# Performance work log

Measured on AMD Instinct MI355X. Metric: run time of the kernel, lower is better.

The kernel has to match this reference:

```python
import jax, jax.numpy as jnp
import numpy as np

HEAD_DIM = 128
SCALE = HEAD_DIM ** -0.5  # head_scaling == up_scaling == 1/sqrt(head_dim)


def setup_inputs() -> dict:
    key = jax.random.key(0)
    kq, kk, ku, kv = jax.random.split(key, 4)
    B, H, S, D = 2, 16, 2048, 128
    Hk, I = 4, 2048
    Q = jax.random.normal(kq, (B, H, S, D), dtype=jnp.float32)
    K = jax.random.normal(kk, (Hk, I, D), dtype=jnp.float32)
    U = jax.random.normal(ku, (Hk, I, D), dtype=jnp.float32)
    V = jax.random.normal(kv, (Hk, I, D), dtype=jnp.float32)
    return {"Q": Q, "K": K, "U": U, "V": V}


def reference(Q, K, U, V):
    # Q: (B, H, S, D); K/U/V: (Hk, I, D); GQA grouping G = H // Hk
    B, H, S, D = Q.shape
    Hk, I, _ = K.shape
    G = H // Hk
    Qr = Q.reshape(B, Hk, G, S, D)
    # gate scores and up projection, both scaled by 1/sqrt(D)
    M = jnp.einsum('bkgsd,kid->bkgsi', Qr, K) * SCALE
    N = jnp.einsum('bkgsd,kid->bkgsi', Qr, U) * SCALE
    A = jax.nn.silu(M) * N  # gated activation, (B, Hk, G, S, I)
    out = jnp.einsum('bkgsi,kid->bkgsd', A, V)
    return out.reshape(B, H, S, D)
```

## Files before the change

### kernel.cpp

```cpp
#include <hip/hip_runtime.h>

#define B_   2
#define H_   16
#define G_   4
#define S_   2048
#define D_   128
#define I_   2048

#define BM   256
#define BN   64
#define TPB  512
#define NIT  (I_ / BN)
#define TSZ  8192

#define KIDX(r,c) ((r)*128 + ((c) ^ (((r)&15)<<3)))
#define VIDX(d,c) ((d)*64  + ((c) ^ (((d)&7)<<3)))

static constexpr float SCALE = 0.08838834764831845f;

typedef __fp16   p2v  __attribute__((ext_vector_type(2)));
typedef _Float16 h8v  __attribute__((ext_vector_type(8)));
typedef float    f4v  __attribute__((ext_vector_type(4)));
typedef float    f16v __attribute__((ext_vector_type(16)));
typedef int      i4v  __attribute__((ext_vector_type(4)));

__device__ __forceinline__ int pkf16(float a, float b) {
    p2v t = __builtin_amdgcn_cvt_pkrtz(a, b);
    int r; __builtin_memcpy(&r, &t, 4); return r;
}

#define GL_LDS(gp, lp) __builtin_amdgcn_global_load_lds(                      \
    (const __attribute__((address_space(1))) void*)(gp),                      \
    (__attribute__((address_space(3))) void*)(lp), 16, 0, 0)

__global__ __launch_bounds__(256) void convert_kernel(
    const float* __restrict__ Kg, const float* __restrict__ Ug,
    const float* __restrict__ Vg, _Float16* __restrict__ ws)
{
    const int bid = blockIdx.x;
    const int tid = threadIdx.x;
    __shared__ float vt[64 * 128];
    if (bid < 256) {
        const int kh = bid >> 6, m = (bid >> 5) & 1, it = bid & 31;
        const float* src = (m ? Ug : Kg) + (size_t)kh * I_ * D_ + (size_t)it * BN * D_;
        _Float16* dst = ws + (((size_t)kh * 3 + m) * 32 + it) * TSZ;
        const int r   = tid >> 2;
        const int cb  = (tid & 3) * 32;
        const int swz = (r & 15) << 3;
#pragma unroll
        for (int g = 0; g < 4; ++g) {
            const int cc0 = cb + g * 8;
            const int d0  = cc0 ^ swz;
            const float4 a = *(const float4*)(src + r * D_ + d0);
            const float4 c = *(const float4*)(src + r * D_ + d0 + 4);
            h8v v; p2v* v2 = (p2v*)&v;
            v2[0] = __builtin_amdgcn_cvt_pkrtz(a.x, a.y);
            v2[1] = __builtin_amdgcn_cvt_pkrtz(a.z, a.w);
            v2[2] = __builtin_amdgcn_cvt_pkrtz(c.x, c.y);
            v2[3] = __builtin_amdgcn_cvt_pkrtz(c.z, c.w);
            *(h8v*)(dst + r * 128 + cc0) = v;
        }
    } else {
        const int v  = bid - 256;
        const int kh = v >> 5, it = v & 31;
        const float* src = Vg + (size_t)kh * I_ * D_ + (size_t)it * BN * D_;
#pragma unroll
        for (int p = 0; p < 8; ++p) {
            const int idx = p * 256 + tid;
            const int i   = idx >> 5;
            const int d4  = (idx & 31) * 4;
            *(float4*)(&vt[i * 128 + d4]) = *(const float4*)(src + (size_t)i * D_ + d4);
        }
        __syncthreads();
        _Float16* dst = ws + (((size_t)kh * 3 + 2) * 32 + it) * TSZ;
        const int d   = tid >> 1;
        const int cb  = (tid & 1) * 32;
        const int swz = (d & 7) << 3;
#pragma unroll
        for (int g = 0; g < 4; ++g) {
            const int cc0 = cb + g * 8;
            const int ib  = cc0 ^ swz;
            h8v w; p2v* w2 = (p2v*)&w;
#pragma unroll
            for (int pr = 0; pr < 4; ++pr)
                w2[pr] = __builtin_amdgcn_cvt_pkrtz(vt[(ib + 2 * pr) * 128 + d],
                                                    vt[(ib + 2 * pr + 1) * 128 + d]);
            *(h8v*)(dst + d * 64 + cc0) = w;
        }
    }
}

__global__ __launch_bounds__(TPB, 2) void flashmlp_kernel(
    const float* __restrict__ Qg, const _Float16* __restrict__ ws,
    float* __restrict__ Og)
{
    __shared__ _Float16 Ks[2 * TSZ];
    __shared__ _Float16 Us[2 * TSZ];
    __shared__ _Float16 Vt[2 * TSZ];

    const int bid   = blockIdx.x;
    const int xcd   = bid & 7;
    const int kh    = xcd >> 1;
    const int j     = ((bid >> 3) << 1) | (xcd & 1);
    const int stile = j & 7;
    const int bg    = j >> 3;
    const int b     = bg >> 2;
    const int g     = bg & 3;
    const int h     = kh * G_ + g;

    const int tid  = threadIdx.x;
    const int wave = tid >> 6;
    const int lane = tid & 63;
    const int l31  = lane & 31;
    const int hl   = lane >> 5;

    const size_t qbase = ((size_t)(b * H_ + h) * S_ + (size_t)stile * BM) * D_;
    const _Float16* wsK = ws + (size_t)kh * 3 * 32 * TSZ;
    const _Float16* wsU = wsK + (size_t)32 * TSZ;
    const _Float16* wsV = wsK + (size_t)64 * TSZ;

    const int so = wave * 1024 + lane * 8;
    const int su = wave * 1024;

    h8v qf[8];
    {
        const float* qp = Qg + qbase + (size_t)(wave * 32 + l31) * D_;
#pragma unroll
        for (int ks = 0; ks < 8; ++ks) {
            const float4 a = *(const float4*)(qp + ks * 16 + hl * 8);
            const float4 c = *(const float4*)(qp + ks * 16 + hl * 8 + 4);
            h8v v; p2v* v2 = (p2v*)&v;
            v2[0] = __builtin_amdgcn_cvt_pkrtz(a.x * SCALE, a.y * SCALE);
            v2[1] = __builtin_amdgcn_cvt_pkrtz(a.z * SCALE, a.w * SCALE);
            v2[2] = __builtin_amdgcn_cvt_pkrtz(c.x * SCALE, c.y * SCALE);
            v2[3] = __builtin_amdgcn_cvt_pkrtz(c.z * SCALE, c.w * SCALE);
            qf[ks] = v;
        }
    }

    f16v acc_o[4];
#pragma unroll
    for (int dt = 0; dt < 4; ++dt)
#pragma unroll
        for (int e = 0; e < 16; ++e)
            acc_o[dt][e] = 0.f;

    {
        GL_LDS(wsK + so,       Ks + su);
        GL_LDS(wsK + so + 512, Ks + su + 512);
        GL_LDS(wsU + so,       Us + su);
        GL_LDS(wsU + so + 512, Us + su + 512);
        GL_LDS(wsV + so,       Vt + su);
        GL_LDS(wsV + so + 512, Vt + su + 512);
    }
    __syncthreads();

    for (int it = 0; it < NIT; ++it) {
        const int cur = it & 1;
        const _Float16* ksb = Ks + cur * TSZ;
        const _Float16* usb = Us + cur * TSZ;
        const _Float16* vtb = Vt + cur * TSZ;

        if (it + 1 < NIT) {
            const int nb = (cur ^ 1) * TSZ;
            const _Float16* kt = wsK + (size_t)(it + 1) * TSZ;
            const _Float16* ut = wsU + (size_t)(it + 1) * TSZ;
            const _Float16* vt = wsV + (size_t)(it + 1) * TSZ;
            GL_LDS(kt + so,       Ks + nb + su);
            GL_LDS(kt + so + 512, Ks + nb + su + 512);
            GL_LDS(ut + so,       Us + nb + su);
            GL_LDS(ut + so + 512, Us + nb + su + 512);
            GL_LDS(vt + so,       Vt + nb + su);
            GL_LDS(vt + so + 512, Vt + nb + su + 512);
        }

#pragma unroll
        for (int t2 = 0; t2 < 2; ++t2) {
            f16v am, an;
#pragma unroll
            for (int e = 0; e < 16; ++e) { am[e] = 0.f; an[e] = 0.f; }
            __builtin_amdgcn_s_setprio(1);
#pragma unroll
            for (int ks = 0; ks < 8; ++ks) {
                const h8v kf = *(const h8v*)(&ksb[KIDX(t2 * 32 + l31, ks * 16 + hl * 8)]);
                const h8v uf = *(const h8v*)(&usb[KIDX(t2 * 32 + l31, ks * 16 + hl * 8)]);
                am = __builtin_amdgcn_mfma_f32_32x32x16_f16(kf, qf[ks], am, 0, 0, 0);
                an = __builtin_amdgcn_mfma_f32_32x32x16_f16(uf, qf[ks], an, 0, 0, 0);
            }
            __builtin_amdgcn_s_setprio(0);

            int P[8];
#pragma unroll
            for (int p = 0; p < 8; ++p) {
                const float m0 = am[2 * p + 0], n0 = an[2 * p + 0];
                const float m1 = am[2 * p + 1], n1 = an[2 * p + 1];
                const float g0 = m0 * __builtin_amdgcn_rcpf(1.f + __expf(-m0)) * n0;
                const float g1 = m1 * __builtin_amdgcn_rcpf(1.f + __expf(-m1)) * n1;
                P[p] = pkf16(g0, g1);
            }
            auto sA = __builtin_amdgcn_permlane32_swap(P[0], P[2], false, false);
            auto sB = __builtin_amdgcn_permlane32_swap(P[1], P[3], false, false);
            auto sC = __builtin_amdgcn_permlane32_swap(P[4], P[6], false, false);
            auto sD = __builtin_amdgcn_permlane32_swap(P[5], P[7], false, false);
            h8v pb0, pb1;
            {
                i4v wlo = i4v{static_cast<int>(sA[0]), static_cast<int>(sB[0]),
                              static_cast<int>(sA[1]), static_cast<int>(sB[1])};
                i4v whi = i4v{static_cast<int>(sC[0]), static_cast<int>(sD[0]),
                              static_cast<int>(sC[1]), static_cast<int>(sD[1])};
                __builtin_memcpy(&pb0, &wlo, 16);
                __builtin_memcpy(&pb1, &whi, 16);
            }

#pragma unroll
            for (int k2 = 0; k2 < 2; ++k2) {
                const int ks2 = t2 * 2 + k2;
                const h8v pb = k2 ? pb1 : pb0;
                h8v va[4];
#pragma unroll
                for (int dt = 0; dt < 4; ++dt)
                    va[dt] = *(const h8v*)(&vtb[VIDX(dt * 32 + l31, ks2 * 16 + hl * 8)]);
                __builtin_amdgcn_s_setprio(1);
#pragma unroll
                for (int dt = 0; dt < 4; ++dt)
                    acc_o[dt] = __builtin_amdgcn_mfma_f32_32x32x16_f16(va[dt], pb, acc_o[dt], 0, 0, 0);
                __builtin_amdgcn_s_setprio(0);
            }
        }

        __syncthreads();
    }

    {
        const int qrow = stile * BM + wave * 32 + l31;
        float* op = Og + ((size_t)(b * H_ + h) * S_ + qrow) * D_;
#pragma unroll
        for (int dt = 0; dt < 4; ++dt)
#pragma unroll
            for (int g4 = 0; g4 < 4; ++g4) {
                f4v v = f4v{acc_o[dt][4 * g4 + 0], acc_o[dt][4 * g4 + 1],
                            acc_o[dt][4 * g4 + 2], acc_o[dt][4 * g4 + 3]};
                *(f4v*)(op + dt * 32 + g4 * 8 + hl * 4) = v;
            }
    }
}

extern "C" void kernel_launch(void* const* d_in, const int* in_sizes, int n_in,
                              void* d_out, int out_size, void* d_ws, size_t ws_size,
                              hipStream_t stream) {
    const float* Q = (const float*)d_in[0];
    const float* K = (const float*)d_in[1];
    const float* U = (const float*)d_in[2];
    const float* V = (const float*)d_in[3];
    float* out = (float*)d_out;
    _Float16* ws = (_Float16*)d_ws;

    convert_kernel<<<dim3(384), dim3(256), 0, stream>>>(K, U, V, ws);
    flashmlp_kernel<<<dim3((S_ / BM) * B_ * H_), dim3(TPB), 0, stream>>>(Q, ws, out);
}
```

Measured before the change: 197.6 us.

## Halve block tiles and split K/U and V pipelines at different granularities

```diff
diff --git a/kernel.cpp b/kernel.cpp
--- a/kernel.cpp
+++ b/kernel.cpp
@@ -7,11 +7,13 @@
 #define D_   128
 #define I_   2048
 
-#define BM   256
-#define BN   64
-#define TPB  512
+#define BM   128
+#define BN   32
+#define TPB  256
 #define NIT  (I_ / BN)
-#define TSZ  8192
+#define KUT  4096
+#define VT   8192
+#define HSTR (3 * 262144)
 
 #define KIDX(r,c) ((r)*128 + ((c) ^ (((r)&15)<<3)))
 #define VIDX(d,c) ((d)*64  + ((c) ^ (((d)&7)<<3)))
@@ -42,11 +44,12 @@
     __shared__ float vt[64 * 128];
     if (bid < 256) {
         const int kh = bid >> 6, m = (bid >> 5) & 1, it = bid & 31;
-        const float* src = (m ? Ug : Kg) + (size_t)kh * I_ * D_ + (size_t)it * BN * D_;
-        _Float16* dst = ws + (((size_t)kh * 3 + m) * 32 + it) * TSZ;
+        const float* src = (m ? Ug : Kg) + (size_t)kh * I_ * D_ + (size_t)it * 64 * D_;
+        _Float16* dstb = ws + (size_t)kh * HSTR + (size_t)m * 262144 + (size_t)it * 2 * KUT;
         const int r   = tid >> 2;
         const int cb  = (tid & 3) * 32;
         const int swz = (r & 15) << 3;
+        _Float16* dst = dstb + (size_t)(r >> 5) * KUT + (r & 31) * 128;
 #pragma unroll
         for (int g = 0; g < 4; ++g) {
             const int cc0 = cb + g * 8;
@@ -58,12 +61,12 @@
             v2[1] = __builtin_amdgcn_cvt_pkrtz(a.z, a.w);
             v2[2] = __builtin_amdgcn_cvt_pkrtz(c.x, c.y);
             v2[3] = __builtin_amdgcn_cvt_pkrtz(c.z, c.w);
-            *(h8v*)(dst + r * 128 + cc0) = v;
+            *(h8v*)(dst + cc0) = v;
         }
     } else {
         const int v  = bid - 256;
         const int kh = v >> 5, it = v & 31;
-        const float* src = Vg + (size_t)kh * I_ * D_ + (size_t)it * BN * D_;
+        const float* src = Vg + (size_t)kh * I_ * D_ + (size_t)it * 64 * D_;
 #pragma unroll
         for (int p = 0; p < 8; ++p) {
             const int idx = p * 256 + tid;
@@ -72,7 +75,7 @@
             *(float4*)(&vt[i * 128 + d4]) = *(const float4*)(src + (size_t)i * D_ + d4);
         }
         __syncthreads();
-        _Float16* dst = ws + (((size_t)kh * 3 + 2) * 32 + it) * TSZ;
+        _Float16* dst = ws + (size_t)kh * HSTR + 2 * 262144 + (size_t)it * VT;
         const int d   = tid >> 1;
         const int cb  = (tid & 1) * 32;
         const int swz = (d & 7) << 3;
@@ -94,16 +97,16 @@
     const float* __restrict__ Qg, const _Float16* __restrict__ ws,
     float* __restrict__ Og)
 {
-    __shared__ _Float16 Ks[2 * TSZ];
-    __shared__ _Float16 Us[2 * TSZ];
-    __shared__ _Float16 Vt[2 * TSZ];
+    __shared__ _Float16 Ks[2 * KUT];
+    __shared__ _Float16 Us[2 * KUT];
+    __shared__ _Float16 Vt[2 * VT];
 
     const int bid   = blockIdx.x;
     const int xcd   = bid & 7;
     const int kh    = xcd >> 1;
     const int j     = ((bid >> 3) << 1) | (xcd & 1);
-    const int stile = j & 7;
-    const int bg    = j >> 3;
+    const int stile = j & 15;
+    const int bg    = j >> 4;
     const int b     = bg >> 2;
     const int g     = bg & 3;
     const int h     = kh * G_ + g;
@@ -115,12 +118,14 @@
     const int hl   = lane >> 5;
 
     const size_t qbase = ((size_t)(b * H_ + h) * S_ + (size_t)stile * BM) * D_;
-    const _Float16* wsK = ws + (size_t)kh * 3 * 32 * TSZ;
-    const _Float16* wsU = wsK + (size_t)32 * TSZ;
-    const _Float16* wsV = wsK + (size_t)64 * TSZ;
-
-    const int so = wave * 1024 + lane * 8;
-    const int su = wave * 1024;
+    const _Float16* wsK = ws + (size_t)kh * HSTR;
+    const _Float16* wsU = wsK + 262144;
+    const _Float16* wsV = wsK + 2 * 262144;
+
+    const int soK = wave * 1024 + lane * 8;
+    const int suK = wave * 1024;
+    const int soV = wave * 2048 + lane * 8;
+    const int suV = wave * 2048;
 
     h8v qf[8];
     {
@@ -146,86 +151,90 @@
             acc_o[dt][e] = 0.f;
 
     {
-        GL_LDS(wsK + so,       Ks + su);
-        GL_LDS(wsK + so + 512, Ks + su + 512);
-        GL_LDS(wsU + so,       Us + su);
-        GL_LDS(wsU + so + 512, Us + su + 512);
-        GL_LDS(wsV + so,       Vt + su);
-        GL_LDS(wsV + so + 512, Vt + su + 512);
+        GL_LDS(wsK + soK,       Ks + suK);
+        GL_LDS(wsK + soK + 512, Ks + suK + 512);
+        GL_LDS(wsU + soK,       Us + suK);
+        GL_LDS(wsU + soK + 512, Us + suK + 512);
+        GL_LDS(wsV + soV,        Vt + suV);
+        GL_LDS(wsV + soV + 512,  Vt + suV + 512);
+        GL_LDS(wsV + soV + 1024, Vt + suV + 1024);
+        GL_LDS(wsV + soV + 1536, Vt + suV + 1536);
     }
     __syncthreads();
 
     for (int it = 0; it < NIT; ++it) {
-        const int cur = it & 1;
-        const _Float16* ksb = Ks + cur * TSZ;
-        const _Float16* usb = Us + cur * TSZ;
-        const _Float16* vtb = Vt + cur * TSZ;
+        const _Float16* ksb = Ks + (it & 1) * KUT;
+        const _Float16* usb = Us + (it & 1) * KUT;
+        const _Float16* vtb = Vt + ((it >> 1) & 1) * VT;
 
         if (it + 1 < NIT) {
-            const int nb = (cur ^ 1) * TSZ;
-            const _Float16* kt = wsK + (size_t)(it + 1) * TSZ;
-            const _Float16* ut = wsU + (size_t)(it + 1) * TSZ;
-            const _Float16* vt = wsV + (size_t)(it + 1) * TSZ;
-            GL_LDS(kt + so,       Ks + nb + su);
-            GL_LDS(kt + so + 512, Ks + nb + su + 512);
-            GL_LDS(ut + so,       Us + nb + su);
-            GL_LDS(ut + so + 512, Us + nb + su + 512);
-            GL_LDS(vt + so,       Vt + nb + su);
-            GL_LDS(vt + so + 512, Vt + nb + su + 512);
-        }
-
-#pragma unroll
-        for (int t2 = 0; t2 < 2; ++t2) {
-            f16v am, an;
-#pragma unroll
-            for (int e = 0; e < 16; ++e) { am[e] = 0.f; an[e] = 0.f; }
+            const int nb = ((it + 1) & 1) * KUT;
+            const _Float16* kt = wsK + (size_t)(it + 1) * KUT;
+            const _Float16* ut = wsU + (size_t)(it + 1) * KUT;
+            GL_LDS(kt + soK,       Ks + nb + suK);
+            GL_LDS(kt + soK + 512, Ks + nb + suK + 512);
+            GL_LDS(ut + soK,       Us + nb + suK);
+            GL_LDS(ut + soK + 512, Us + nb + suK + 512);
+        }
+        if (!(it & 1) && (it >> 1) + 1 < 32) {
+            const int vb = (it >> 1) + 1;
+            const _Float16* vt = wsV + (size_t)vb * VT;
+            const int nv = (vb & 1) * VT;
+            GL_LDS(vt + soV,        Vt + nv + suV);
+            GL_LDS(vt + soV + 512,  Vt + nv + suV + 512);
+            GL_LDS(vt + soV + 1024, Vt + nv + suV + 1024);
+            GL_LDS(vt + soV + 1536, Vt + nv + suV + 1536);
+        }
+
+        f16v am, an;
+#pragma unroll
+        for (int e = 0; e < 16; ++e) { am[e] = 0.f; an[e] = 0.f; }
+        __builtin_amdgcn_s_setprio(1);
+#pragma unroll
+        for (int ks = 0; ks < 8; ++ks) {
+            const h8v kf = *(const h8v*)(&ksb[KIDX(l31, ks * 16 + hl * 8)]);
+            const h8v uf = *(const h8v*)(&usb[KIDX(l31, ks * 16 + hl * 8)]);
+            am = __builtin_amdgcn_mfma_f32_32x32x16_f16(kf, qf[ks], am, 0, 0, 0);
+            an = __builtin_amdgcn_mfma_f32_32x32x16_f16(uf, qf[ks], an, 0, 0, 0);
+        }
+        __builtin_amdgcn_s_setprio(0);
+
+        int P[8];
+#pragma unroll
+        for (int p = 0; p < 8; ++p) {
+            const float m0 = am[2 * p + 0], n0 = an[2 * p + 0];
+            const float m1 = am[2 * p + 1], n1 = an[2 * p + 1];
+            const float g0 = m0 * __builtin_amdgcn_rcpf(1.f + __expf(-m0)) * n0;
+            const float g1 = m1 * __builtin_amdgcn_rcpf(1.f + __expf(-m1)) * n1;
+            P[p] = pkf16(g0, g1);
+        }
+        auto sA = __builtin_amdgcn_permlane32_swap(P[0], P[2], false, false);
+        auto sB = __builtin_amdgcn_permlane32_swap(P[1], P[3], false, false);
+        auto sC = __builtin_amdgcn_permlane32_swap(P[4], P[6], false, false);
+        auto sD = __builtin_amdgcn_permlane32_swap(P[5], P[7], false, false);
+        h8v pb0, pb1;
+        {
+            i4v wlo = i4v{static_cast<int>(sA[0]), static_cast<int>(sB[0]),
+                          static_cast<int>(sA[1]), static_cast<int>(sB[1])};
+            i4v whi = i4v{static_cast<int>(sC[0]), static_cast<int>(sD[0]),
+                          static_cast<int>(sC[1]), static_cast<int>(sD[1])};
+            __builtin_memcpy(&pb0, &wlo, 16);
+            __builtin_memcpy(&pb1, &whi, 16);
+        }
+
+#pragma unroll
+        for (int k2 = 0; k2 < 2; ++k2) {
+            const int ks2 = (it & 1) * 2 + k2;
+            const h8v pb = k2 ? pb1 : pb0;
+            h8v va[4];
+#pragma unroll
+            for (int dt = 0; dt < 4; ++dt)
+                va[dt] = *(const h8v*)(&vtb[VIDX(dt * 32 + l31, ks2 * 16 + hl * 8)]);
             __builtin_amdgcn_s_setprio(1);
 #pragma unroll
-            for (int ks = 0; ks < 8; ++ks) {
-                const h8v kf = *(const h8v*)(&ksb[KIDX(t2 * 32 + l31, ks * 16 + hl * 8)]);
-                const h8v uf = *(const h8v*)(&usb[KIDX(t2 * 32 + l31, ks * 16 + hl * 8)]);
-                am = __builtin_amdgcn_mfma_f32_32x32x16_f16(kf, qf[ks], am, 0, 0, 0);
-                an = __builtin_amdgcn_mfma_f32_32x32x16_f16(uf, qf[ks], an, 0, 0, 0);
-            }
+            for (int dt = 0; dt < 4; ++dt)
+                acc_o[dt] = __builtin_amdgcn_mfma_f32_32x32x16_f16(va[dt], pb, acc_o[dt], 0, 0, 0);
             __builtin_amdgcn_s_setprio(0);
-
-            int P[8];
-#pragma unroll
-            for (int p = 0; p < 8; ++p) {
-                const float m0 = am[2 * p + 0], n0 = an[2 * p + 0];
-                const float m1 = am[2 * p + 1], n1 = an[2 * p + 1];
-                const float g0 = m0 * __builtin_amdgcn_rcpf(1.f + __expf(-m0)) * n0;
-                const float g1 = m1 * __builtin_amdgcn_rcpf(1.f + __expf(-m1)) * n1;
-                P[p] = pkf16(g0, g1);
-            }
-            auto sA = __builtin_amdgcn_permlane32_swap(P[0], P[2], false, false);
-            auto sB = __builtin_amdgcn_permlane32_swap(P[1], P[3], false, false);
-            auto sC = __builtin_amdgcn_permlane32_swap(P[4], P[6], false, false);
-            auto sD = __builtin_amdgcn_permlane32_swap(P[5], P[7], false, false);
-            h8v pb0, pb1;
-            {
-                i4v wlo = i4v{static_cast<int>(sA[0]), static_cast<int>(sB[0]),
-                              static_cast<int>(sA[1]), static_cast<int>(sB[1])};
-                i4v whi = i4v{static_cast<int>(sC[0]), static_cast<int>(sD[0]),
-                              static_cast<int>(sC[1]), static_cast<int>(sD[1])};
-                __builtin_memcpy(&pb0, &wlo, 16);
-                __builtin_memcpy(&pb1, &whi, 16);
-            }
-
-#pragma unroll
-            for (int k2 = 0; k2 < 2; ++k2) {
-                const int ks2 = t2 * 2 + k2;
-                const h8v pb = k2 ? pb1 : pb0;
-                h8v va[4];
-#pragma unroll
-                for (int dt = 0; dt < 4; ++dt)
-                    va[dt] = *(const h8v*)(&vtb[VIDX(dt * 32 + l31, ks2 * 16 + hl * 8)]);
-                __builtin_amdgcn_s_setprio(1);
-#pragma unroll
-                for (int dt = 0; dt < 4; ++dt)
-                    acc_o[dt] = __builtin_amdgcn_mfma_f32_32x32x16_f16(va[dt], pb, acc_o[dt], 0, 0, 0);
-                __builtin_amdgcn_s_setprio(0);
-            }
         }
 
         __syncthreads();
```

Measured after the change: 201.6 us. 2.0% more time.
